# Optimization experiments

Hardware: AMD Instinct MI355X
Metric: run time of the kernel (lower is better)

The kernel has to match this reference:

```python
import jax, jax.numpy as jnp
import numpy as np


def setup_inputs() -> dict:
    key = jax.random.key(0)
    ks = jax.random.split(key, 6)
    B, H, W, C = 2, 96, 96, 64
    x = jax.random.normal(ks[0], (B, H, W, C), dtype=jnp.float32)
    # 1x1 conv weights as [C_in, C_out] matrices (kernel size 1)
    W1 = jax.random.normal(ks[1], (C, C // 8), dtype=jnp.float32) * 0.1
    b1 = jnp.zeros((C // 8,), dtype=jnp.float32)
    W2 = jax.random.normal(ks[2], (C, C // 8), dtype=jnp.float32) * 0.1
    b2 = jnp.zeros((C // 8,), dtype=jnp.float32)
    W3 = jax.random.normal(ks[3], (C, C // 2), dtype=jnp.float32) * 0.1
    b3 = jnp.zeros((C // 2,), dtype=jnp.float32)
    W4 = jax.random.normal(ks[4], (C // 2, C), dtype=jnp.float32) * 0.1
    b4 = jnp.zeros((C,), dtype=jnp.float32)
    gamma = jax.random.uniform(ks[5], (1,), dtype=jnp.float32)
    return {"x": x, "W1": W1, "b1": b1, "W2": W2, "b2": b2,
            "W3": W3, "b3": b3, "W4": W4, "b4": b4, "gamma": gamma}


def reference(x, W1, b1, W2, b2, W3, b3, W4, b4, gamma):
    B, H, W_, C = x.shape
    N = H * W_
    # 1x1 convs == per-pixel matmuls
    f = jnp.einsum('bhwc,cd->bhwd', x, W1) + b1   # [B,H,W,C/8] (key)
    g = jnp.einsum('bhwc,cd->bhwd', x, W2) + b2   # [B,H,W,C/8] (query)
    h = jnp.einsum('bhwc,cd->bhwd', x, W3) + b3   # [B,H,W,C/2] (value)
    f = f.reshape(B, N, -1)
    g = g.reshape(B, N, -1)
    h = h.reshape(B, N, -1)
    s = jnp.einsum('bnd,bmd->bnm', g, f)          # [B,N,N] full score matrix
    beta = jax.nn.softmax(s, axis=-1)
    o = jnp.einsum('bnm,bmd->bnd', beta, h)       # [B,N,C/2]
    o = o.reshape(B, H, W_, C // 2)
    o = jnp.einsum('bhwc,cd->bhwd', o, W4) + b4   # [B,H,W,C]
    return gamma[0] * o + x
```

## Files before the change

kernel.cpp:

```cpp
#include <hip/hip_runtime.h>
#include <hip/hip_bf16.h>


#define BATCH 2
#define NTOK 9216
#define CCH 64
#define DV 32
#define KS 4
#define KEYS_PER_BLOCK (NTOK / KS)
#define KEYS_PER_WAVE (KEYS_PER_BLOCK / 2)
#define KT 32
#define NKT (KEYS_PER_WAVE / KT)
#define ROWS (BATCH * NTOK)
#define QT (ROWS / 32)
#define LOG2E 1.44269504088896340736f
#define PB 32

typedef __attribute__((ext_vector_type(8))) short bf16x8;
typedef __attribute__((ext_vector_type(4))) float f32x4;

__device__ __forceinline__ short f2bf(float x) {
    __hip_bfloat16 h = __float2bfloat16(x);
    return *(short*)&h;
}
__device__ __forceinline__ float bf2f(short s) {
    unsigned u = ((unsigned)(unsigned short)s) << 16;
    return *(float*)&u;
}

__global__ __launch_bounds__(512) void proj_kernel(
    const float* __restrict__ x,
    const float* __restrict__ W1, const float* __restrict__ b1,
    const float* __restrict__ W2, const float* __restrict__ b2,
    const float* __restrict__ W3, const float* __restrict__ b3,
    short* __restrict__ fx, short* __restrict__ gx, short* __restrict__ hT,
    float4* __restrict__ zbase)
{
    __shared__ float xS[PB][CCH];
    __shared__ short fgS[2][PB][32];
    __shared__ short hS[32][PB + 2];

    const int tid = threadIdx.x;
    const int r0  = blockIdx.x * PB;

    if (tid < 264) zbase[blockIdx.x * 264 + tid] = make_float4(0.f, 0.f, 0.f, 0.f);

    ((float4*)xS)[tid] = ((const float4*)(x + (size_t)r0 * CCH))[tid];
    __syncthreads();

    {
        const int rr = tid >> 4;
        const int c  = tid & 15;
        const float* xr = xS[rr];
        if (c < 8) {
            float acc = b1[c];
            #pragma unroll
            for (int k = 0; k < CCH; ++k) acc += xr[k] * W1[k * 8 + c];
            short hi = f2bf(acc);
            short lo = f2bf(acc - bf2f(hi));
            fgS[0][rr][c] = hi; fgS[0][rr][c + 8] = hi;
            fgS[0][rr][c + 16] = lo; fgS[0][rr][c + 24] = 0;
        } else {
            const int cc = c - 8;
            float acc = b2[cc];
            #pragma unroll
            for (int k = 0; k < CCH; ++k) acc += xr[k] * W2[k * 8 + cc];
            acc *= LOG2E;
            short hi = f2bf(acc);
            short lo = f2bf(acc - bf2f(hi));
            fgS[1][rr][cc] = hi; fgS[1][rr][cc + 8] = lo;
            fgS[1][rr][cc + 16] = hi; fgS[1][rr][cc + 24] = 0;
        }
    }
    {
        const int c = tid & 31;
        const int rbase = tid >> 5;
        #pragma unroll
        for (int s = 0; s < 2; ++s) {
            int rr = rbase + s * 16;
            float acc = b3[c];
            #pragma unroll
            for (int k = 0; k < CCH; ++k) acc += xS[rr][k] * W3[k * 32 + c];
            int np = ((rr & 15) >> 2) * 8 + (rr & 3) + ((rr >> 4) & 1) * 4;
            hS[c][np] = f2bf(acc);
        }
    }
    __syncthreads();

    ((int*)(fx + (size_t)r0 * 32))[tid] = ((const int*)fgS[0])[tid];
    ((int*)(gx + (size_t)r0 * 32))[tid] = ((const int*)fgS[1])[tid];
    {
        const int b  = r0 / NTOK;
        const int n0 = r0 - b * NTOK;
        const int c  = tid >> 4;
        const int d  = tid & 15;
        ((int*)(hT + (size_t)(b * 32 + c) * NTOK + n0))[d] = ((const int*)&hS[c][0])[d];
    }
}

__global__ __launch_bounds__(128, 4) void attn_kernel(
    const short* __restrict__ fx, const short* __restrict__ gx,
    const short* __restrict__ hT,
    float* __restrict__ l_acc, float* __restrict__ o_acc)
{
    __shared__ float red[32 * 33];

    const int tid  = threadIdx.x;
    const int wave = tid >> 6;
    const int lane = tid & 63;
    const int col  = lane & 15;
    const int quad = lane >> 4;

    const int blk = blockIdx.x;
    const int qt  = blk % QT;
    const int ks  = blk / QT;
    const int b   = qt / (QT / BATCH);
    const int qbase   = (qt % (QT / BATCH)) * 32;
    const int rowbase = b * NTOK + qbase;

    const bf16x8 agA = *(const bf16x8*)(gx + (size_t)(rowbase + col) * 32 + quad * 8);
    const bf16x8 agB = *(const bf16x8*)(gx + (size_t)(rowbase + 16 + col) * 32 + quad * 8);

    f32x4 oA0 = {0.f,0.f,0.f,0.f}, oA1 = {0.f,0.f,0.f,0.f};
    f32x4 oB0 = {0.f,0.f,0.f,0.f}, oB1 = {0.f,0.f,0.f,0.f};
    float lA = 0.f, lB = 0.f;
    const f32x4 zero4 = {0.f,0.f,0.f,0.f};

    const int kstart = ks * KEYS_PER_BLOCK + wave * KEYS_PER_WAVE;
    const short* fbase = fx + ((size_t)b * NTOK + kstart) * 32;
    const short* hp0 = hT + ((size_t)(b * 32 + col)) * NTOK + kstart;
    const short* hp1 = hT + ((size_t)(b * 32 + 16 + col)) * NTOK + kstart;

    bf16x8 fa0 = *(const bf16x8*)(fbase + (size_t)col * 32 + quad * 8);
    bf16x8 fa1 = *(const bf16x8*)(fbase + (size_t)(16 + col) * 32 + quad * 8);
    bf16x8 hb0 = *(const bf16x8*)(hp0 + quad * 8);
    bf16x8 hb1 = *(const bf16x8*)(hp1 + quad * 8);

    union PU { int i[4]; bf16x8 v; };

    for (int t = 0; t < NKT; ++t) {
        f32x4 t00 = __builtin_amdgcn_mfma_f32_16x16x32_bf16(fa0, agA, zero4, 0, 0, 0);
        f32x4 t01 = __builtin_amdgcn_mfma_f32_16x16x32_bf16(fa1, agA, zero4, 0, 0, 0);
        f32x4 t10 = __builtin_amdgcn_mfma_f32_16x16x32_bf16(fa0, agB, zero4, 0, 0, 0);
        f32x4 t11 = __builtin_amdgcn_mfma_f32_16x16x32_bf16(fa1, agB, zero4, 0, 0, 0);

        const int kn = (t + 1 < NKT) ? (t + 1) * KT : 0;
        bf16x8 nf0 = *(const bf16x8*)(fbase + (size_t)(kn + col) * 32 + quad * 8);
        bf16x8 nf1 = *(const bf16x8*)(fbase + (size_t)(kn + 16 + col) * 32 + quad * 8);
        bf16x8 nh0 = *(const bf16x8*)(hp0 + kn + quad * 8);
        bf16x8 nh1 = *(const bf16x8*)(hp1 + kn + quad * 8);

        PU pA, pB;
        {
            float e0 = __builtin_amdgcn_exp2f(t00[0]), e1 = __builtin_amdgcn_exp2f(t00[1]);
            float e2 = __builtin_amdgcn_exp2f(t00[2]), e3 = __builtin_amdgcn_exp2f(t00[3]);
            float e4 = __builtin_amdgcn_exp2f(t01[0]), e5 = __builtin_amdgcn_exp2f(t01[1]);
            float e6 = __builtin_amdgcn_exp2f(t01[2]), e7 = __builtin_amdgcn_exp2f(t01[3]);
            lA += (e0 + e1) + (e2 + e3) + (e4 + e5) + (e6 + e7);
            pA.i[0] = (int)__builtin_amdgcn_perm((unsigned)__float_as_int(e1) + 0x8000u,
                                                 (unsigned)__float_as_int(e0) + 0x8000u, 0x07060302u);
            pA.i[1] = (int)__builtin_amdgcn_perm((unsigned)__float_as_int(e3) + 0x8000u,
                                                 (unsigned)__float_as_int(e2) + 0x8000u, 0x07060302u);
            pA.i[2] = (int)__builtin_amdgcn_perm((unsigned)__float_as_int(e5) + 0x8000u,
                                                 (unsigned)__float_as_int(e4) + 0x8000u, 0x07060302u);
            pA.i[3] = (int)__builtin_amdgcn_perm((unsigned)__float_as_int(e7) + 0x8000u,
                                                 (unsigned)__float_as_int(e6) + 0x8000u, 0x07060302u);
        }
        {
            float e0 = __builtin_amdgcn_exp2f(t10[0]), e1 = __builtin_amdgcn_exp2f(t10[1]);
            float e2 = __builtin_amdgcn_exp2f(t10[2]), e3 = __builtin_amdgcn_exp2f(t10[3]);
            float e4 = __builtin_amdgcn_exp2f(t11[0]), e5 = __builtin_amdgcn_exp2f(t11[1]);
            float e6 = __builtin_amdgcn_exp2f(t11[2]), e7 = __builtin_amdgcn_exp2f(t11[3]);
            lB += (e0 + e1) + (e2 + e3) + (e4 + e5) + (e6 + e7);
            pB.i[0] = (int)__builtin_amdgcn_perm((unsigned)__float_as_int(e1) + 0x8000u,
                                                 (unsigned)__float_as_int(e0) + 0x8000u, 0x07060302u);
            pB.i[1] = (int)__builtin_amdgcn_perm((unsigned)__float_as_int(e3) + 0x8000u,
                                                 (unsigned)__float_as_int(e2) + 0x8000u, 0x07060302u);
            pB.i[2] = (int)__builtin_amdgcn_perm((unsigned)__float_as_int(e5) + 0x8000u,
                                                 (unsigned)__float_as_int(e4) + 0x8000u, 0x07060302u);
            pB.i[3] = (int)__builtin_amdgcn_perm((unsigned)__float_as_int(e7) + 0x8000u,
                                                 (unsigned)__float_as_int(e6) + 0x8000u, 0x07060302u);
        }

        oA0 = __builtin_amdgcn_mfma_f32_16x16x32_bf16(pA.v, hb0, oA0, 0, 0, 0);
        oA1 = __builtin_amdgcn_mfma_f32_16x16x32_bf16(pA.v, hb1, oA1, 0, 0, 0);
        oB0 = __builtin_amdgcn_mfma_f32_16x16x32_bf16(pB.v, hb0, oB0, 0, 0, 0);
        oB1 = __builtin_amdgcn_mfma_f32_16x16x32_bf16(pB.v, hb1, oB1, 0, 0, 0);

        fa0 = nf0; fa1 = nf1; hb0 = nh0; hb1 = nh1;
    }

    lA += __shfl_xor(lA, 16); lA += __shfl_xor(lA, 32);
    lB += __shfl_xor(lB, 16); lB += __shfl_xor(lB, 32);

    if (wave == 1) {
        #pragma unroll
        for (int r = 0; r < 4; ++r) {
            red[(quad * 4 + r) * 33 + col]           = oA0[r];
            red[(quad * 4 + r) * 33 + 16 + col]      = oA1[r];
            red[(16 + quad * 4 + r) * 33 + col]      = oB0[r];
            red[(16 + quad * 4 + r) * 33 + 16 + col] = oB1[r];
        }
        if (quad == 0) {
            red[col * 33 + 32]        = lA;
            red[(16 + col) * 33 + 32] = lB;
        }
    }
    __syncthreads();
    if (wave == 0) {
        #pragma unroll
        for (int r = 0; r < 4; ++r) {
            int qA = quad * 4 + r, qB = 16 + quad * 4 + r;
            atomicAdd(&o_acc[(size_t)(rowbase + qA) * 32 + col],      oA0[r] + red[qA * 33 + col]);
            atomicAdd(&o_acc[(size_t)(rowbase + qA) * 32 + 16 + col], oA1[r] + red[qA * 33 + 16 + col]);
            atomicAdd(&o_acc[(size_t)(rowbase + qB) * 32 + col],      oB0[r] + red[qB * 33 + col]);
            atomicAdd(&o_acc[(size_t)(rowbase + qB) * 32 + 16 + col], oB1[r] + red[qB * 33 + 16 + col]);
        }
        if (quad == 0) {
            atomicAdd(&l_acc[rowbase + col],      lA + red[col * 33 + 32]);
            atomicAdd(&l_acc[rowbase + 16 + col], lB + red[(16 + col) * 33 + 32]);
        }
    }
}

__global__ __launch_bounds__(256) void merge_kernel(
    const float* __restrict__ l_acc, const float* __restrict__ o_acc,
    const float* __restrict__ x,
    const float* __restrict__ W4, const float* __restrict__ b4,
    const float* __restrict__ gamma, float* __restrict__ out)
{
    __shared__ float oS[4][DV];
    int wave = threadIdx.x >> 6;
    int lane = threadIdx.x & 63;
    int row  = blockIdx.x * 4 + wave;

    float invL = 1.f / l_acc[row];
    if (lane < DV) {
        oS[wave][lane] = o_acc[(size_t)row * DV + lane] * invL;
    }
    __syncthreads();

    float dot = b4[lane];
    #pragma unroll
    for (int k = 0; k < DV; ++k) dot += oS[wave][k] * W4[k * 64 + lane];
    float gm  = gamma[0];
    float res = x[(size_t)row * 64 + lane];
    out[(size_t)row * 64 + lane] = gm * dot + res;
}

extern "C" void kernel_launch(void* const* d_in, const int* in_sizes, int n_in,
                              void* d_out, int out_size, void* d_ws, size_t ws_size,
                              hipStream_t stream) {
    const float* x     = (const float*)d_in[0];
    const float* W1    = (const float*)d_in[1];
    const float* b1    = (const float*)d_in[2];
    const float* W2    = (const float*)d_in[3];
    const float* b2    = (const float*)d_in[4];
    const float* W3    = (const float*)d_in[5];
    const float* b3    = (const float*)d_in[6];
    const float* W4    = (const float*)d_in[7];
    const float* b4    = (const float*)d_in[8];
    const float* gamma = (const float*)d_in[9];
    float* out = (float*)d_out;

    short* fx    = (short*)d_ws;
    short* gx    = fx + (size_t)ROWS * 32;
    short* hT    = gx + (size_t)ROWS * 32;
    float* l_acc = (float*)(hT + (size_t)ROWS * 32);
    float* o_acc = l_acc + ROWS;

    proj_kernel<<<ROWS / PB, 512, 0, stream>>>(
        x, W1, b1, W2, b2, W3, b3, fx, gx, hT, (float4*)l_acc);

    attn_kernel<<<QT * KS, 128, 0, stream>>>(fx, gx, hT, l_acc, o_acc);

    merge_kernel<<<ROWS / 4, 256, 0, stream>>>(l_acc, o_acc, x, W4, b4, gamma, out);
}
```

Measured before the change: 154.9 us.

## Split attention keys across four waves per block and de-diverge projection

The attention kernel now runs four waves per block instead of two. Each wave handles a quarter of the block's key range, and the partial outputs and row sums of waves 1-3 are reduced through three shared-memory buffers before wave 0 does the atomics. This doubles the number of waves available to hide memory and MFMA latency, at the cost of more shared memory and a tighter register budget under launch_bounds(256,8), which could cause spills. Separately, the projection kernel maps threads so that each wave computes either the f projection or the g projection, which removes intra-wave branch divergence.

Result: slower. 159.6 us (+3.0%).

```diff
diff --git a/kernel.cpp b/kernel.cpp
--- a/kernel.cpp
+++ b/kernel.cpp
@@ -8,7 +8,7 @@
 #define DV 32
 #define KS 4
 #define KEYS_PER_BLOCK (NTOK / KS)
-#define KEYS_PER_WAVE (KEYS_PER_BLOCK / 2)
+#define KEYS_PER_WAVE (KEYS_PER_BLOCK / 4)
 #define KT 32
 #define NKT (KEYS_PER_WAVE / KT)
 #define ROWS (BATCH * NTOK)
@@ -49,10 +49,11 @@
     __syncthreads();
 
     {
-        const int rr = tid >> 4;
-        const int c  = tid & 15;
+        const int half = tid >> 8;
+        const int rr   = (tid & 255) >> 3;
+        const int c    = tid & 7;
         const float* xr = xS[rr];
-        if (c < 8) {
+        if (half == 0) {
             float acc = b1[c];
             #pragma unroll
             for (int k = 0; k < CCH; ++k) acc += xr[k] * W1[k * 8 + c];
@@ -61,15 +62,14 @@
             fgS[0][rr][c] = hi; fgS[0][rr][c + 8] = hi;
             fgS[0][rr][c + 16] = lo; fgS[0][rr][c + 24] = 0;
         } else {
-            const int cc = c - 8;
-            float acc = b2[cc];
+            float acc = b2[c];
             #pragma unroll
-            for (int k = 0; k < CCH; ++k) acc += xr[k] * W2[k * 8 + cc];
+            for (int k = 0; k < CCH; ++k) acc += xr[k] * W2[k * 8 + c];
             acc *= LOG2E;
             short hi = f2bf(acc);
             short lo = f2bf(acc - bf2f(hi));
-            fgS[1][rr][cc] = hi; fgS[1][rr][cc + 8] = lo;
-            fgS[1][rr][cc + 16] = hi; fgS[1][rr][cc + 24] = 0;
+            fgS[1][rr][c] = hi; fgS[1][rr][c + 8] = lo;
+            fgS[1][rr][c + 16] = hi; fgS[1][rr][c + 24] = 0;
         }
     }
     {
@@ -98,12 +98,12 @@
     }
 }
 
-__global__ __launch_bounds__(128, 4) void attn_kernel(
+__global__ __launch_bounds__(256, 8) void attn_kernel(
     const short* __restrict__ fx, const short* __restrict__ gx,
     const short* __restrict__ hT,
     float* __restrict__ l_acc, float* __restrict__ o_acc)
 {
-    __shared__ float red[32 * 33];
+    __shared__ float red[3][32 * 33];
 
     const int tid  = threadIdx.x;
     const int wave = tid >> 6;
@@ -193,17 +193,18 @@
     lA += __shfl_xor(lA, 16); lA += __shfl_xor(lA, 32);
     lB += __shfl_xor(lB, 16); lB += __shfl_xor(lB, 32);
 
-    if (wave == 1) {
+    if (wave >= 1) {
+        float* rw = red[wave - 1];
         #pragma unroll
         for (int r = 0; r < 4; ++r) {
-            red[(quad * 4 + r) * 33 + col]           = oA0[r];
-            red[(quad * 4 + r) * 33 + 16 + col]      = oA1[r];
-            red[(16 + quad * 4 + r) * 33 + col]      = oB0[r];
-            red[(16 + quad * 4 + r) * 33 + 16 + col] = oB1[r];
+            rw[(quad * 4 + r) * 33 + col]           = oA0[r];
+            rw[(quad * 4 + r) * 33 + 16 + col]      = oA1[r];
+            rw[(16 + quad * 4 + r) * 33 + col]      = oB0[r];
+            rw[(16 + quad * 4 + r) * 33 + 16 + col] = oB1[r];
         }
         if (quad == 0) {
-            red[col * 33 + 32]        = lA;
-            red[(16 + col) * 33 + 32] = lB;
+            rw[col * 33 + 32]        = lA;
+            rw[(16 + col) * 33 + 32] = lB;
         }
     }
     __syncthreads();
@@ -211,14 +212,20 @@
         #pragma unroll
         for (int r = 0; r < 4; ++r) {
             int qA = quad * 4 + r, qB = 16 + quad * 4 + r;
-            atomicAdd(&o_acc[(size_t)(rowbase + qA) * 32 + col],      oA0[r] + red[qA * 33 + col]);
-            atomicAdd(&o_acc[(size_t)(rowbase + qA) * 32 + 16 + col], oA1[r] + red[qA * 33 + 16 + col]);
-            atomicAdd(&o_acc[(size_t)(rowbase + qB) * 32 + col],      oB0[r] + red[qB * 33 + col]);
-            atomicAdd(&o_acc[(size_t)(rowbase + qB) * 32 + 16 + col], oB1[r] + red[qB * 33 + 16 + col]);
+            float vA0 = oA0[r] + red[0][qA * 33 + col]      + red[1][qA * 33 + col]      + red[2][qA * 33 + col];
+            float vA1 = oA1[r] + red[0][qA * 33 + 16 + col] + red[1][qA * 33 + 16 + col] + red[2][qA * 33 + 16 + col];
+            float vB0 = oB0[r] + red[0][qB * 33 + col]      + red[1][qB * 33 + col]      + red[2][qB * 33 + col];
+            float vB1 = oB1[r] + red[0][qB * 33 + 16 + col] + red[1][qB * 33 + 16 + col] + red[2][qB * 33 + 16 + col];
+            atomicAdd(&o_acc[(size_t)(rowbase + qA) * 32 + col],      vA0);
+            atomicAdd(&o_acc[(size_t)(rowbase + qA) * 32 + 16 + col], vA1);
+            atomicAdd(&o_acc[(size_t)(rowbase + qB) * 32 + col],      vB0);
+            atomicAdd(&o_acc[(size_t)(rowbase + qB) * 32 + 16 + col], vB1);
         }
         if (quad == 0) {
-            atomicAdd(&l_acc[rowbase + col],      lA + red[col * 33 + 32]);
-            atomicAdd(&l_acc[rowbase + 16 + col], lB + red[(16 + col) * 33 + 32]);
+            float tA = lA + red[0][col * 33 + 32] + red[1][col * 33 + 32] + red[2][col * 33 + 32];
+            float tB = lB + red[0][(16 + col) * 33 + 32] + red[1][(16 + col) * 33 + 32] + red[2][(16 + col) * 33 + 32];
+            atomicAdd(&l_acc[rowbase + col],      tA);
+            atomicAdd(&l_acc[rowbase + 16 + col], tB);
         }
     }
 }
@@ -272,7 +279,7 @@
     proj_kernel<<<ROWS / PB, 512, 0, stream>>>(
         x, W1, b1, W2, b2, W3, b3, fx, gx, hT, (float4*)l_acc);
 
-    attn_kernel<<<QT * KS, 128, 0, stream>>>(fx, gx, hT, l_acc, o_acc);
+    attn_kernel<<<QT * KS, 256, 0, stream>>>(fx, gx, hT, l_acc, o_acc);
 
     merge_kernel<<<ROWS / 4, 256, 0, stream>>>(l_acc, o_acc, x, W4, b4, gamma, out);
 }
```
